# Kernel tuning notes

Hardware: AMD Instinct MI355X
Metric: run time of the kernel (lower is better)

Reference implementation:

```python
import jax, jax.numpy as jnp
import numpy as np

A, B, D, L = 256, 64, 768, 2  # annotators, batch, hidden, num_labels
G1, G2 = 4, 8                 # groups per attribute


def setup_inputs() -> dict:
    key = jax.random.key(0)
    ks = jax.random.split(key, 9)
    s = 1.0 / np.sqrt(D)
    return {
        "pooled": jax.random.normal(ks[0], (B, D), jnp.float32),
        "W1": jax.random.normal(ks[1], (G1, D, D), jnp.float32) * s,
        "b1": jax.random.normal(ks[2], (G1, D), jnp.float32) * s,
        "W2": jax.random.normal(ks[3], (G2, D, D), jnp.float32) * s,
        "b2": jax.random.normal(ks[4], (G2, D), jnp.float32) * s,
        "Wh": jax.random.normal(ks[5], (A, D, L), jnp.float32) * s,
        "bh": jax.random.normal(ks[6], (A, L), jnp.float32) * s,
        "g1_idx": jax.random.randint(ks[7], (A,), 0, G1),
        "g2_idx": jax.random.randint(ks[8], (A,), 0, G2),
    }


def reference(pooled, W1, b1, W2, b2, Wh, bh, g1_idx, g2_idx):
    # Attribute 1: every annotator with the same group shares the transform,
    # so compute once per group then gather (avoids A redundant GEMMs).
    h_g = jnp.einsum('bd,gde->gbe', pooled, W1) + b1[:, None, :]   # [G1, B, D]
    h = h_g[g1_idx]                                                # [A, B, D]
    # Attribute 2: input now differs per annotator -> grouped GEMM via gathered weights.
    h = jnp.einsum('abd,ade->abe', h, W2[g2_idx]) + b2[g2_idx][:, None, :]  # [A, B, D]
    # Per-annotator classification heads.
    logits = jnp.einsum('abd,adl->abl', h, Wh) + bh[:, None, :]    # [A, B, L]
    # Match torch layout: logits[batch, annotator, label]
    return jnp.transpose(logits, (1, 0, 2))                        # [B, A, L]
```

## Files before the change

kernel.cpp:

```cpp
#include <hip/hip_runtime.h>

#define AN 256
#define BN 64
#define DN 768
#define LN 2
#define G1N 4
#define G2N 8
#define KI (DN / 32)
#define PAD 776

typedef __attribute__((ext_vector_type(8))) short short8;
typedef __attribute__((ext_vector_type(4))) short bf16x4;
typedef __attribute__((ext_vector_type(4))) float floatx4;

static __device__ __forceinline__ unsigned short f2bf(float f) {
    union { float f; unsigned int u; } v; v.f = f;
    unsigned int r = v.u + 0x7FFF + ((v.u >> 16) & 1);
    return (unsigned short)(r >> 16);
}
static __device__ __forceinline__ unsigned int pack2(float a, float b) {
    return (unsigned int)f2bf(a) | ((unsigned int)f2bf(b) << 16);
}

__global__ __launch_bounds__(256) void k_main(
    const float* __restrict__ pooled, const float* __restrict__ W1,
    const float* __restrict__ b1, const float* __restrict__ W2,
    const float* __restrict__ b2, const float* __restrict__ Wh,
    const float* __restrict__ bh, const int* __restrict__ g2i,
    unsigned short* __restrict__ h1, unsigned short* __restrict__ Wcs,
    float* __restrict__ bc)
{
    __shared__ __align__(16) unsigned char smem[49664];
    const int tid = threadIdx.x, bx = blockIdx.x;
    const int lane = tid & 63, wave = tid >> 6;
    const int nn = lane & 15, quad = lane >> 4;

    if (bx < 96) {
        unsigned short* Wt = (unsigned short*)smem;
        const int g = bx / 24, e0 = (bx % 24) * 32;
        const float* src = W1 + (size_t)g * DN * DN + e0;
        const int dr = tid >> 3, q8 = tid & 7;

        #pragma unroll
        for (int round = 0; round < 24; ++round) {
            const int d = round * 32 + dr;
            float4 v = *(const float4*)(src + (size_t)d * DN + q8 * 4);
            Wt[(q8 * 4 + 0) * PAD + d] = f2bf(v.x);
            Wt[(q8 * 4 + 1) * PAD + d] = f2bf(v.y);
            Wt[(q8 * 4 + 2) * PAD + d] = f2bf(v.z);
            Wt[(q8 * 4 + 3) * PAD + d] = f2bf(v.w);
        }
        __syncthreads();

        const int mt = wave;
        const float* Ap = pooled + (size_t)(mt * 16 + nn) * DN + quad * 8;
        floatx4 acc0 = {0, 0, 0, 0}, acc1 = {0, 0, 0, 0};
        #pragma unroll
        for (int kk = 0; kk < KI; ++kk) {
            float4 a0 = *(const float4*)(Ap + kk * 32);
            float4 a1 = *(const float4*)(Ap + kk * 32 + 4);
            short8 af;
            af[0] = (short)f2bf(a0.x); af[1] = (short)f2bf(a0.y);
            af[2] = (short)f2bf(a0.z); af[3] = (short)f2bf(a0.w);
            af[4] = (short)f2bf(a1.x); af[5] = (short)f2bf(a1.y);
            af[6] = (short)f2bf(a1.z); af[7] = (short)f2bf(a1.w);
            short8 bf0 = *(const short8*)(Wt + (size_t)nn * PAD + kk * 32 + quad * 8);
            short8 bf1 = *(const short8*)(Wt + (size_t)(16 + nn) * PAD + kk * 32 + quad * 8);
            acc0 = __builtin_amdgcn_mfma_f32_16x16x32_bf16(af, bf0, acc0, 0, 0, 0);
            acc1 = __builtin_amdgcn_mfma_f32_16x16x32_bf16(af, bf1, acc1, 0, 0, 0);
        }

        const float bv0 = b1[g * DN + e0 + nn];
        const float bv1 = b1[g * DN + e0 + 16 + nn];
        unsigned short* hrow = h1 + (size_t)g * BN * DN;
        #pragma unroll
        for (int rr = 0; rr < 4; ++rr) {
            const size_t ro = (size_t)(mt * 16 + quad * 4 + rr) * DN;
            hrow[ro + e0 + nn]      = f2bf(acc0[rr] + bv0);
            hrow[ro + e0 + 16 + nn] = f2bf(acc1[rr] + bv1);
        }
    } else if (bx < 192) {
        int* g2s  = (int*)smem;
        int* lst2 = (int*)(smem + 1024);
        unsigned short* Whs = (unsigned short*)(smem + 2048);

        const int j = bx - 96, g = j / 12, mbase = (j % 12) * 64;

        const int m_row = mbase + wave * 16 + nn;
        const float* ap = W2 + ((size_t)g * DN + m_row) * DN + quad * 8;
        short8 Areg[KI];
        #pragma unroll
        for (int kk = 0; kk < KI; ++kk) {
            float4 a0 = *(const float4*)(ap + kk * 32);
            float4 a1 = *(const float4*)(ap + kk * 32 + 4);
            short8 af;
            af[0] = (short)f2bf(a0.x); af[1] = (short)f2bf(a0.y);
            af[2] = (short)f2bf(a0.z); af[3] = (short)f2bf(a0.w);
            af[4] = (short)f2bf(a1.x); af[5] = (short)f2bf(a1.y);
            af[6] = (short)f2bf(a1.z); af[7] = (short)f2bf(a1.w);
            Areg[kk] = af;
        }

        g2s[tid] = g2i[tid];
        __syncthreads();
        const int my = g2s[tid];
        int rk = 0;
        for (int a2 = 0; a2 < tid; ++a2) rk += (g2s[a2] == my);
        if (my == g) lst2[rk] = tid;
        int n2g = 0;
        for (int a2 = 0; a2 < AN; ++a2) n2g += (g2s[a2] == g);
        __syncthreads();
        const int cols = 2 * n2g;

        const int al = tid >> 5, t32 = tid & 31;
        for (int c0 = 0; c0 < cols; c0 += 16) {
            const int sidx = (c0 >> 1) + al;
            if (sidx < n2g) {
                const int a = lst2[sidx];
                const float4* wa4 = (const float4*)(Wh + (size_t)a * (DN * LN));
                #pragma unroll
                for (int i = 0; i < 12; ++i) {
                    const int f4 = i * 32 + t32;
                    float4 v = wa4[f4];
                    const int e2 = f4 * 2;
                    *(unsigned int*)(Whs + (2 * al)     * PAD + e2) = pack2(v.x, v.z);
                    *(unsigned int*)(Whs + (2 * al + 1) * PAD + e2) = pack2(v.y, v.w);
                }
            }
            __syncthreads();
            const unsigned short* Brow = Whs + nn * PAD + quad * 8;
            floatx4 acc = {0, 0, 0, 0};
            #pragma unroll
            for (int kk = 0; kk < KI; ++kk) {
                short8 bf = *(const short8*)(Brow + kk * 32);
                acc = __builtin_amdgcn_mfma_f32_16x16x32_bf16(Areg[kk], bf, acc, 0, 0, 0);
            }
            const int c = c0 + nn;
            if (c < cols) {
                const int dbase = mbase + wave * 16 + quad * 4;
                bf16x4 v;
                #pragma unroll
                for (int rr = 0; rr < 4; ++rr) v[rr] = (short)f2bf(acc[rr]);
                *(bf16x4*)(Wcs + (size_t)(g * 256 + c) * DN + dbase) = v;
            }
            __syncthreads();
        }
    } else {
        const int jb = bx - 192;
        const int aa = tid >> 3, jj = tid & 7;
        const int a = jb * 32 + aa;
        const int gv2 = g2i[a];
        const float* whp = Wh + (size_t)a * (DN * LN);
        const float* b2p = b2 + gv2 * DN;
        float acc0 = 0.f, acc1 = 0.f;
        #pragma unroll 4
        for (int i = 0; i < 48; ++i) {
            int e = jj * 96 + i * 2;
            float4 w4 = *(const float4*)(whp + e * 2);
            float2 bv = *(const float2*)(b2p + e);
            acc0 += bv.x * w4.x + bv.y * w4.z;
            acc1 += bv.x * w4.y + bv.y * w4.w;
        }
        #pragma unroll
        for (int off = 4; off; off >>= 1) {
            acc0 += __shfl_down(acc0, off, 64);
            acc1 += __shfl_down(acc1, off, 64);
        }
        if (jj == 0) {
            bc[a * 2 + 0] = acc0 + bh[a * 2 + 0];
            bc[a * 2 + 1] = acc1 + bh[a * 2 + 1];
        }
    }
}

__global__ __launch_bounds__(256) void k_out(
    const unsigned short* __restrict__ h1, const unsigned short* __restrict__ Wcs,
    const float* __restrict__ bc, const int* __restrict__ g1i,
    const int* __restrict__ g2i, float* __restrict__ out)
{
    __shared__ int g1s[AN], g2s[AN], lst1[AN], sx2[AN];
    const int g = blockIdx.y;
    const int tid = threadIdx.x;
    g1s[tid] = g1i[tid];
    g2s[tid] = g2i[tid];
    __syncthreads();
    const int m1 = g1s[tid], m2 = g2s[tid];
    int r1 = 0, r2 = 0;
    for (int a2 = 0; a2 < tid; ++a2) {
        r1 += (g1s[a2] == m1);
        r2 += (g2s[a2] == m2);
    }
    sx2[tid] = r2;
    if (m1 == g) lst1[r1] = tid;
    int n1g = 0;
    for (int a2 = 0; a2 < AN; ++a2) n1g += (g1s[a2] == g);
    __syncthreads();

    const int cols = 2 * n1g;
    const int nt0 = blockIdx.x * 16;
    if (nt0 >= cols) return;

    const int lane = tid & 63, wave = tid >> 6;
    const int nn = lane & 15, quad = lane >> 4;

    const int c = nt0 + nn;
    const bool valid = (c < cols);
    const int cl = valid ? c : (cols - 1);
    const int a = lst1[cl >> 1];
    const int l = cl & 1;
    const int rp = (g2s[a] * 128 + sx2[a]) * 2 + l;

    const unsigned short* hg = h1 + (size_t)g * BN * DN + (size_t)(wave * 16 + nn) * DN + quad * 8;
    const unsigned short* wp = Wcs + (size_t)rp * DN + quad * 8;

    floatx4 acc = {0, 0, 0, 0};
    #pragma unroll
    for (int kk = 0; kk < KI; ++kk) {
        short8 af = *(const short8*)(hg + kk * 32);
        short8 bf = *(const short8*)(wp + kk * 32);
        acc = __builtin_amdgcn_mfma_f32_16x16x32_bf16(af, bf, acc, 0, 0, 0);
    }
    if (valid) {
        const float bv = bc[a * 2 + l];
        #pragma unroll
        for (int r = 0; r < 4; ++r)
            out[(size_t)(wave * 16 + quad * 4 + r) * (AN * LN) + a * 2 + l] = acc[r] + bv;
    }
}

extern "C" void kernel_launch(void* const* d_in, const int* in_sizes, int n_in,
                              void* d_out, int out_size, void* d_ws, size_t ws_size,
                              hipStream_t stream) {
    const float* pooled = (const float*)d_in[0];
    const float* W1     = (const float*)d_in[1];
    const float* b1     = (const float*)d_in[2];
    const float* W2     = (const float*)d_in[3];
    const float* b2     = (const float*)d_in[4];
    const float* Wh     = (const float*)d_in[5];
    const float* bh     = (const float*)d_in[6];
    const int*   g1i    = (const int*)d_in[7];
    const int*   g2i    = (const int*)d_in[8];
    float* out = (float*)d_out;

    char* ws = (char*)d_ws;
    float* bc = (float*)ws;                           ws += 512 * 4;
    unsigned short* h1  = (unsigned short*)ws;        ws += (size_t)G1N * BN * DN * 2;
    unsigned short* Wcs = (unsigned short*)ws;

    dim3 blk(256);
    k_main<<<dim3(200),   blk, 0, stream>>>(pooled, W1, b1, W2, b2, Wh, bh, g2i,
                                            h1, Wcs, bc);
    k_out <<<dim3(32, 4), blk, 0, stream>>>(h1, Wcs, bc, g1i, g2i, out);
}
```

Measured before the change: 117.8 us.

## Stage W2 slice through LDS coalesced and double-buffer Wh head tiles

The W2 slice for each block is now loaded with fully coalesced float4 reads, converted to bf16 into a large LDS buffer, and the MFMA A fragments are then read back from LDS. Before, each lane did strided per-row global loads. The Wh head tiles are double-buffered, so the next tile's global load and conversion overlap the current tile's MFMAs and one barrier per tile is removed. The cost is much larger LDS use (about 148 KB), which limits occupancy to one block per CU, plus an extra LDS round trip.

```diff
diff --git a/kernel.cpp b/kernel.cpp
--- a/kernel.cpp
+++ b/kernel.cpp
@@ -30,7 +30,7 @@
     unsigned short* __restrict__ h1, unsigned short* __restrict__ Wcs,
     float* __restrict__ bc)
 {
-    __shared__ __align__(16) unsigned char smem[49664];
+    __shared__ __align__(16) unsigned char smem[151040];
     const int tid = threadIdx.x, bx = blockIdx.x;
     const int lane = tid & 63, wave = tid >> 6;
     const int nn = lane & 15, quad = lane >> 4;
@@ -80,29 +80,36 @@
             hrow[ro + e0 + 16 + nn] = f2bf(acc1[rr] + bv1);
         }
     } else if (bx < 192) {
-        int* g2s  = (int*)smem;
-        int* lst2 = (int*)(smem + 1024);
-        unsigned short* Whs = (unsigned short*)(smem + 2048);
+        unsigned short* W2s = (unsigned short*)smem;
+        unsigned short* Whs = (unsigned short*)(smem + 99328);
+        int* g2s  = (int*)(smem + 148992);
+        int* lst2 = (int*)(smem + 150016);
 
         const int j = bx - 96, g = j / 12, mbase = (j % 12) * 64;
 
-        const int m_row = mbase + wave * 16 + nn;
-        const float* ap = W2 + ((size_t)g * DN + m_row) * DN + quad * 8;
+        g2s[tid] = g2i[tid];
+        {
+            const float* sl = W2 + ((size_t)g * DN + mbase) * DN;
+            #pragma unroll
+            for (int i = 0; i < 48; ++i) {
+                const int idx = i * 256 + tid;
+                const int r = idx / 192, c4 = idx % 192;
+                float4 v = *(const float4*)(sl + (size_t)r * DN + c4 * 4);
+                bf16x4 b;
+                b[0] = (short)f2bf(v.x); b[1] = (short)f2bf(v.y);
+                b[2] = (short)f2bf(v.z); b[3] = (short)f2bf(v.w);
+                *(bf16x4*)(W2s + (size_t)r * PAD + c4 * 4) = b;
+            }
+        }
+        __syncthreads();
+
         short8 Areg[KI];
-        #pragma unroll
-        for (int kk = 0; kk < KI; ++kk) {
-            float4 a0 = *(const float4*)(ap + kk * 32);
-            float4 a1 = *(const float4*)(ap + kk * 32 + 4);
-            short8 af;
-            af[0] = (short)f2bf(a0.x); af[1] = (short)f2bf(a0.y);
-            af[2] = (short)f2bf(a0.z); af[3] = (short)f2bf(a0.w);
-            af[4] = (short)f2bf(a1.x); af[5] = (short)f2bf(a1.y);
-            af[6] = (short)f2bf(a1.z); af[7] = (short)f2bf(a1.w);
-            Areg[kk] = af;
-        }
-
-        g2s[tid] = g2i[tid];
-        __syncthreads();
+        {
+            const unsigned short* ar = W2s + (size_t)(wave * 16 + nn) * PAD + quad * 8;
+            #pragma unroll
+            for (int kk = 0; kk < KI; ++kk)
+                Areg[kk] = *(const short8*)(ar + kk * 32);
+        }
         const int my = g2s[tid];
         int rk = 0;
         for (int a2 = 0; a2 < tid; ++a2) rk += (g2s[a2] == my);
@@ -111,31 +118,47 @@
         for (int a2 = 0; a2 < AN; ++a2) n2g += (g2s[a2] == g);
         __syncthreads();
         const int cols = 2 * n2g;
+        const int ntiles = (cols + 15) >> 4;
 
         const int al = tid >> 5, t32 = tid & 31;
-        for (int c0 = 0; c0 < cols; c0 += 16) {
-            const int sidx = (c0 >> 1) + al;
-            if (sidx < n2g) {
+        if (al < n2g) {
+            const int a = lst2[al];
+            const float4* wa4 = (const float4*)(Wh + (size_t)a * (DN * LN));
+            #pragma unroll
+            for (int i = 0; i < 12; ++i) {
+                const int f4 = i * 32 + t32;
+                float4 v = wa4[f4];
+                const int e2 = f4 * 2;
+                *(unsigned int*)(Whs + (size_t)(2 * al)     * PAD + e2) = pack2(v.x, v.z);
+                *(unsigned int*)(Whs + (size_t)(2 * al + 1) * PAD + e2) = pack2(v.y, v.w);
+            }
+        }
+        __syncthreads();
+
+        for (int t = 0; t < ntiles; ++t) {
+            const int cur = t & 1;
+            const unsigned short* Brow = Whs + (size_t)(cur * 16 + nn) * PAD + quad * 8;
+            floatx4 acc = {0, 0, 0, 0};
+            #pragma unroll
+            for (int kk = 0; kk < KI; ++kk) {
+                short8 bf = *(const short8*)(Brow + kk * 32);
+                acc = __builtin_amdgcn_mfma_f32_16x16x32_bf16(Areg[kk], bf, acc, 0, 0, 0);
+            }
+            const int sidx = ((t + 1) << 3) + al;
+            if (t + 1 < ntiles && sidx < n2g) {
                 const int a = lst2[sidx];
                 const float4* wa4 = (const float4*)(Wh + (size_t)a * (DN * LN));
+                unsigned short* dst = Whs + (size_t)((cur ^ 1) * 16) * PAD;
                 #pragma unroll
                 for (int i = 0; i < 12; ++i) {
                     const int f4 = i * 32 + t32;
                     float4 v = wa4[f4];
                     const int e2 = f4 * 2;
-                    *(unsigned int*)(Whs + (2 * al)     * PAD + e2) = pack2(v.x, v.z);
-                    *(unsigned int*)(Whs + (2 * al + 1) * PAD + e2) = pack2(v.y, v.w);
+                    *(unsigned int*)(dst + (size_t)(2 * al)     * PAD + e2) = pack2(v.x, v.z);
+                    *(unsigned int*)(dst + (size_t)(2 * al + 1) * PAD + e2) = pack2(v.y, v.w);
                 }
             }
-            __syncthreads();
-            const unsigned short* Brow = Whs + nn * PAD + quad * 8;
-            floatx4 acc = {0, 0, 0, 0};
-            #pragma unroll
-            for (int kk = 0; kk < KI; ++kk) {
-                short8 bf = *(const short8*)(Brow + kk * 32);
-                acc = __builtin_amdgcn_mfma_f32_16x16x32_bf16(Areg[kk], bf, acc, 0, 0, 0);
-            }
-            const int c = c0 + nn;
+            const int c = t * 16 + nn;
             if (c < cols) {
                 const int dbase = mbase + wave * 16 + quad * 4;
                 bf16x4 v;
```

Result: no change. 117.8 us (-0.1%).
